# Kernel optimization log

Hardware: AMD Instinct MI355X
Metric: run time of the kernel (lower is better)

The kernel has to match this reference:

```python
import jax, jax.numpy as jnp
import numpy as np

N_HEAD = 8
DROP_RATE = 0.1


def setup_inputs() -> dict:
    key = jax.random.key(0)
    k1, k2, k3 = jax.random.split(key, 3)
    n, c, h, w = 16, 512, 32, 32
    return {
        "x": jax.random.normal(k1, (n, c, h, w), jnp.float32),
        "qkv_w": jax.random.normal(k2, (3 * c, c), jnp.float32) * 0.02,
        "qkv_b": jnp.zeros((3 * c,), jnp.float32),
        "out_w": jax.random.normal(k3, (c, c), jnp.float32) * 0.02,
        "out_b": jnp.zeros((c,), jnp.float32),
        "dropout_enabled": 0,
    }


def reference(x, qkv_w, qkv_b, out_w, out_b, dropout_enabled):
    n, c, h, w = x.shape
    hd = c // N_HEAD  # head dim
    # fused QKV 1x1 conv == per-pixel matmul: [n, 3c, h, w]
    qkv = jnp.einsum('oc,nchw->nohw', qkv_w, x) + qkv_b[None, :, None, None]
    # [n, 3*n_head, hd, h*w] -> [n, 3*n_head, h*w, hd]
    qkv = jnp.swapaxes(qkv.reshape(n, N_HEAD * 3, hd, h * w), 2, 3)
    q, k, v = jnp.split(qkv, 3, axis=1)  # each [n, n_head, hw, hd]
    scale = hd ** (-0.25)
    att = jax.nn.softmax((q * scale) @ (jnp.swapaxes(k, 2, 3) * scale), axis=3)
    y = jnp.swapaxes(att @ v, 2, 3).reshape(n, c, h, w)
    y = jnp.einsum('oc,nchw->nohw', out_w, y) + out_b[None, :, None, None]
    # Dropout2d: drops whole (n, c) channel maps
    rate = DROP_RATE * dropout_enabled
    keep = jax.random.bernoulli(jax.random.key(42), 1.0 - rate, shape=(n, c))
    y = y * keep[..., None, None] / (1.0 - rate)
    return x + y
```

## Files before the change

### kernel.cpp

```cpp
#include <hip/hip_runtime.h>

typedef short bf16x8 __attribute__((ext_vector_type(8)));
typedef float f32x4 __attribute__((ext_vector_type(4)));
typedef float f32x16 __attribute__((ext_vector_type(16)));

#define MFMA16(a,b,c) __builtin_amdgcn_mfma_f32_16x16x32_bf16((a),(b),(c),0,0,0)
#define MFMA32(a,b,c) __builtin_amdgcn_mfma_f32_32x32x16_bf16((a),(b),(c),0,0,0)

static __device__ __forceinline__ unsigned short f2bf(float f){
  unsigned u; __builtin_memcpy(&u, &f, 4);
  u += 0x7fffu + ((u >> 16) & 1u);
  return (unsigned short)(u >> 16);
}

static __device__ __forceinline__ unsigned cvtpk(float lo, float hi){
  unsigned r;
  asm volatile("v_cvt_pk_bf16_f32 %0, %1, %2" : "=v"(r) : "v"(lo), "v"(hi));
  return r;
}
static __device__ __forceinline__ void pl32swap(unsigned &a, unsigned &b){
  asm volatile("v_permlane32_swap_b32 %0, %1" : "+v"(a), "+v"(b));
}

static __device__ __forceinline__ void gload_lds16(const void* g, void* l) {
  __builtin_amdgcn_global_load_lds(
      (__attribute__((address_space(1))) void*)g,
      (__attribute__((address_space(3))) void*)l, 16, 0, 0);
}

__global__ __launch_bounds__(256) void cvt_w(
    const float* __restrict__ qkv_w, const float* __restrict__ out_w,
    unsigned short* __restrict__ wq, unsigned short* __restrict__ wo) {
  int i = blockIdx.x * 256 + threadIdx.x;
  if (i < 786432) wq[i] = f2bf(qkv_w[i]);
  else            wo[i - 786432] = f2bf(out_w[i - 786432]);
}

__global__ __launch_bounds__(256) void transpose_cvt(
    const float* __restrict__ in, unsigned short* __restrict__ out)
{
  __shared__ unsigned short tile[32][33];
  const long base = (long)blockIdx.z * 512 * 1024;
  const int t = threadIdx.x, tx = t & 31, ty = t >> 5;
  const int c0 = blockIdx.x * 32, r0 = blockIdx.y * 32;
  const float* ib = in + base;
#pragma unroll
  for (int i = 0; i < 4; ++i)
    tile[ty + i * 8][tx] = f2bf(ib[(long)(r0 + ty + i * 8) * 1024 + c0 + tx]);
  __syncthreads();
  unsigned short* ob = out + base;
#pragma unroll
  for (int i = 0; i < 4; ++i)
    ob[(long)(c0 + ty + i * 8) * 512 + r0 + tx] = tile[tx][ty + i * 8];
}

__global__ __launch_bounds__(256, 2) void gemm_qkv(
    const unsigned short* __restrict__ A, const unsigned short* __restrict__ B,
    unsigned short* __restrict__ qkvout, const float* __restrict__ bias)
{
  const int M = 1024, K = 512;
  __shared__ unsigned short SM[4][128 * 64];
  const int t = threadIdx.x, lane = t & 63, wv = t >> 6;
  const int quad = lane >> 4, ln = lane & 15;

  const int L = blockIdx.x + 12 * blockIdx.y + 96 * blockIdx.z;
  const int v = (L & 7) * 192 + (L >> 3);
  const int m0 = ((v / 12) & 7) * 128, n0 = (v % 12) * 128;
  const long zb = v / 96;
  A += zb * (long)M * K;

  const int srow = wv * 32 + (lane >> 3);
  const int scol = ((lane & 7) * 8) ^ ((lane >> 3) * 8);

  auto stage = [&](int kt, unsigned short* Ad, unsigned short* Bd) {
#pragma unroll
    for (int i = 0; i < 4; ++i) {
      gload_lds16(&A[(long)(m0 + srow + i * 8) * K + kt + scol],
                  &Ad[(wv * 32 + i * 8) * 64]);
      gload_lds16(&B[(long)(n0 + srow + i * 8) * K + kt + scol],
                  &Bd[(wv * 32 + i * 8) * 64]);
    }
  };

  f32x4 zero = {0.f, 0.f, 0.f, 0.f};
  f32x4 acc[4][4];
#pragma unroll
  for (int i = 0; i < 4; ++i)
#pragma unroll
    for (int j = 0; j < 4; ++j) acc[i][j] = zero;

  const int wm = (wv & 1) * 64, wn = (wv >> 1) * 64;
  const int rsw = (ln & 7) * 8;

  stage(0, SM[0], SM[2]);
  for (int kt8 = 0; kt8 < 8; ++kt8) {
    const int cur = kt8 & 1;
    if (kt8 < 7) {
      stage((kt8 + 1) * 64, SM[cur ^ 1], SM[2 + (cur ^ 1)]);
      asm volatile("s_waitcnt vmcnt(8)" ::: "memory");
    } else {
      asm volatile("s_waitcnt vmcnt(0)" ::: "memory");
    }
    __builtin_amdgcn_s_barrier();
    const unsigned short* As = SM[cur];
    const unsigned short* Bs = SM[2 + cur];
#pragma unroll
    for (int kk = 0; kk < 64; kk += 32) {
      bf16x8 a[4], b[4];
#pragma unroll
      for (int i = 0; i < 4; ++i)
        a[i] = *(const bf16x8*)&As[(wm + i * 16 + ln) * 64 + ((kk + quad * 8) ^ rsw)];
#pragma unroll
      for (int j = 0; j < 4; ++j)
        b[j] = *(const bf16x8*)&Bs[(wn + j * 16 + ln) * 64 + ((kk + quad * 8) ^ rsw)];
#pragma unroll
      for (int i = 0; i < 4; ++i)
#pragma unroll
        for (int j = 0; j < 4; ++j)
          acc[i][j] = MFMA16(a[i], b[j], acc[i][j]);
    }
    __builtin_amdgcn_s_barrier();
  }

  const int part = n0 >> 9;
  if (part < 2) {
    const float qs = (part == 0) ? 0.18033688f : 1.0f;
    unsigned short (*T)[136] = (unsigned short(*)[136])&SM[0][0];
    __syncthreads();
#pragma unroll
    for (int j = 0; j < 4; ++j) {
      const int oo = wn + j * 16 + ln;
      const float bb = bias[n0 + oo];
#pragma unroll
      for (int i = 0; i < 4; ++i) {
        const int pp = wm + i * 16 + quad * 4;
        f32x4 vv = acc[i][j];
#pragma unroll
        for (int r = 0; r < 4; ++r)
          T[pp + r][oo] = f2bf((vv[r] + bb) * qs);
      }
    }
    __syncthreads();
    unsigned short* qb = qkvout + (long)part * 8388608;
#pragma unroll
    for (int it = 0; it < 8; ++it) {
      const int idx = it * 256 + t;
      const int p = idx >> 4, c0 = (idx & 15) * 8;
      const int og = n0 + c0;
      const int h = (og >> 6) & 7, d = og & 63;
      bf16x8 val = *(const bf16x8*)&T[p][c0];
      *(bf16x8*)&qb[((long)(zb * 8 + h) * 1024 + m0 + p) * 64 + d] = val;
    }
  } else {
#pragma unroll
    for (int j = 0; j < 4; ++j) {
      const int o = n0 + wn + j * 16 + ln;
      const float bb = bias[o];
#pragma unroll
      for (int i = 0; i < 4; ++i) {
        const int p = m0 + wm + i * 16 + quad * 4;
        const long cidx = ((long)zb * 512 + (o - 1024)) * 1024 + p;
        f32x4 vv = acc[i][j];
        ushort4 st;
        st.x = f2bf(vv[0] + bb); st.y = f2bf(vv[1] + bb);
        st.z = f2bf(vv[2] + bb); st.w = f2bf(vv[3] + bb);
        *(ushort4*)&qkvout[16777216 + cidx] = st;
      }
    }
  }
}

__global__ __launch_bounds__(256, 2) void gemm_out(
    const unsigned short* __restrict__ A, const unsigned short* __restrict__ B,
    float* __restrict__ C, const float* __restrict__ bias,
    const float* __restrict__ xin, const int* __restrict__ de_ptr)
{
  const int M = 1024, K = 512;
  __shared__ unsigned short SM[4][128 * 64];
  const int t = threadIdx.x, lane = t & 63, wv = t >> 6;
  const int quad = lane >> 4, ln = lane & 15;

  const int L = blockIdx.x + 4 * blockIdx.y + 32 * blockIdx.z;
  const int v = (L & 7) * 64 + (L >> 3);
  const int m0 = ((v >> 2) & 7) * 128, n0 = (v & 3) * 128;
  const long zb = v >> 5;
  A += zb * (long)M * K;
  C += zb * 512l * M;
  xin += zb * 512l * M;

  const int srow = wv * 32 + (lane >> 3);
  const int scol = ((lane & 7) * 8) ^ ((lane >> 3) * 8);

  auto stage = [&](int kt, unsigned short* Ad, unsigned short* Bd) {
#pragma unroll
    for (int i = 0; i < 4; ++i) {
      gload_lds16(&A[(long)(m0 + srow + i * 8) * K + kt + scol],
                  &Ad[(wv * 32 + i * 8) * 64]);
      gload_lds16(&B[(long)(n0 + srow + i * 8) * K + kt + scol],
                  &Bd[(wv * 32 + i * 8) * 64]);
    }
  };

  f32x4 zero = {0.f, 0.f, 0.f, 0.f};
  f32x4 acc[4][4];
#pragma unroll
  for (int i = 0; i < 4; ++i)
#pragma unroll
    for (int j = 0; j < 4; ++j) acc[i][j] = zero;

  const int wm = (wv & 1) * 64, wn = (wv >> 1) * 64;
  const int rsw = (ln & 7) * 8;

  stage(0, SM[0], SM[2]);
  for (int kt8 = 0; kt8 < 8; ++kt8) {
    const int cur = kt8 & 1;
    if (kt8 < 7) {
      stage((kt8 + 1) * 64, SM[cur ^ 1], SM[2 + (cur ^ 1)]);
      asm volatile("s_waitcnt vmcnt(8)" ::: "memory");
    } else {
      asm volatile("s_waitcnt vmcnt(0)" ::: "memory");
    }
    __builtin_amdgcn_s_barrier();
    const unsigned short* As = SM[cur];
    const unsigned short* Bs = SM[2 + cur];
#pragma unroll
    for (int kk = 0; kk < 64; kk += 32) {
      bf16x8 a[4], b[4];
#pragma unroll
      for (int i = 0; i < 4; ++i)
        a[i] = *(const bf16x8*)&As[(wm + i * 16 + ln) * 64 + ((kk + quad * 8) ^ rsw)];
#pragma unroll
      for (int j = 0; j < 4; ++j)
        b[j] = *(const bf16x8*)&Bs[(wn + j * 16 + ln) * 64 + ((kk + quad * 8) ^ rsw)];
#pragma unroll
      for (int i = 0; i < 4; ++i)
#pragma unroll
        for (int j = 0; j < 4; ++j)
          acc[i][j] = MFMA16(a[i], b[j], acc[i][j]);
    }
    __builtin_amdgcn_s_barrier();
  }

  float dscale = 1.0f / (1.0f - 0.1f * (float)de_ptr[0]);

#pragma unroll
  for (int j = 0; j < 4; ++j) {
    int o = n0 + wn + j * 16 + ln;
    float bb = bias[o];
#pragma unroll
    for (int i = 0; i < 4; ++i) {
      int p = m0 + wm + i * 16 + quad * 4;
      long cidx = (long)o * M + p;
      f32x4 vv = acc[i][j];
      float4 rx = *(const float4*)&xin[cidx];
      float4 st;
      st.x = rx.x + (vv[0] + bb) * dscale;
      st.y = rx.y + (vv[1] + bb) * dscale;
      st.z = rx.z + (vv[2] + bb) * dscale;
      st.w = rx.w + (vv[3] + bb) * dscale;
      *(float4*)&C[cidx] = st;
    }
  }
}

__global__ __launch_bounds__(512, 2) void attn_kernel(
    const unsigned short* __restrict__ q_pd, const unsigned short* __restrict__ k_pd,
    const unsigned short* __restrict__ v_cp, unsigned short* __restrict__ y_pc)
{
  __shared__ unsigned short Ks[3][128 * 64];
  __shared__ unsigned short Vs[3][64 * 128];
  const int t = threadIdx.x, lane = t & 63, wv = t >> 6;
  const int l31 = lane & 31, bh8 = (lane >> 5) * 8;
  const int qt = blockIdx.y >> 5;
  const int nh = blockIdx.x * 32 + (blockIdx.y & 31);
  const int n = nh >> 3, h = nh & 7;
  const int q0 = qt * 512;

  bf16x8 qa[2][4];
#pragma unroll
  for (int qg = 0; qg < 2; ++qg) {
    const unsigned short* qb =
        q_pd + ((long)nh * 1024 + q0 + wv * 64 + qg * 32 + l31) * 64;
#pragma unroll
    for (int ds = 0; ds < 4; ++ds)
      qa[qg][ds] = *(const bf16x8*)(qb + ds * 16 + bh8);
  }

  f32x16 zacc;
#pragma unroll
  for (int r = 0; r < 16; ++r) zacc[r] = 0.f;
  f32x16 o_acc[2][2];
  o_acc[0][0] = zacc; o_acc[0][1] = zacc; o_acc[1][0] = zacc; o_acc[1][1] = zacc;
  float l_acc[2] = {0.f, 0.f};

  const unsigned short* kg0 = k_pd + (long)nh * 1024 * 64;
  const unsigned short* vg0 = v_cp + ((long)n * 512 + h * 64) * 1024;

  const int krow = lane >> 3;
  const int kcol = ((lane & 7) * 8) ^ ((lane >> 3) * 8);
  const int vrow = lane >> 4;
  const int rsw = (lane & 7) * 8;
  const int vrsw = (l31 & 15) * 8;

  auto stage_kv = [&](int c, int buf) {
    const unsigned short* kg = kg0 + (long)c * 128 * 64;
    const unsigned short* vg = vg0 + c * 128;
    unsigned short* KsD = Ks[buf];
    unsigned short* VsD = Vs[buf];
#pragma unroll
    for (int i = 0; i < 2; ++i) {
      const int vr = ((wv & 1) * 8) + i * 4 + vrow;
      const int vcol = ((lane & 15) ^ vr) * 8;
      gload_lds16(kg + (long)(wv * 16 + i * 8 + krow) * 64 + kcol,
                  &KsD[(wv * 16 + i * 8) * 64]);
      gload_lds16(vg + (long)(wv * 8 + i * 4 + vrow) * 1024 + vcol,
                  &VsD[(wv * 8 + i * 4) * 128]);
    }
  };

  stage_kv(0, 0);
  stage_kv(1, 1);

  union U { bf16x8 v; unsigned u[4]; };
  auto sm_pack = [&](const f32x16& sv, bf16x8* paq, float& lac) {
    float e[16];
#pragma unroll
    for (int r = 0; r < 16; ++r) e[r] = __builtin_amdgcn_exp2f(sv[r]);
    float ls = 0.f;
#pragma unroll
    for (int r = 0; r < 16; ++r) ls += e[r];
    lac += ls;
    unsigned pk4[4][2];
#pragma unroll
    for (int hh = 0; hh < 4; ++hh) {
      pk4[hh][0] = cvtpk(e[4 * hh + 0], e[4 * hh + 1]);
      pk4[hh][1] = cvtpk(e[4 * hh + 2], e[4 * hh + 3]);
    }
#pragma unroll
    for (int hk = 0; hk < 2; ++hk) {
      unsigned a0 = pk4[2 * hk + 1][0], b0 = pk4[2 * hk][0];
      unsigned a1 = pk4[2 * hk + 1][1], b1 = pk4[2 * hk][1];
      pl32swap(a0, b0); pl32swap(a1, b1);
      U u; u.u[0] = b0; u.u[1] = b1; u.u[2] = a0; u.u[3] = a1;
      paq[hk] = u.v;
    }
  };

  for (int c = 0; c < 8; ++c) {
    const int cur = c % 3;
    if (c < 6) {
      stage_kv(c + 2, (c + 2) % 3);
      asm volatile("s_waitcnt vmcnt(8)" ::: "memory");
    } else if (c == 6) {
      asm volatile("s_waitcnt vmcnt(4)" ::: "memory");
    } else {
      asm volatile("s_waitcnt vmcnt(0)" ::: "memory");
    }
    __builtin_amdgcn_s_barrier();
    const unsigned short* KsC = Ks[cur];
    const unsigned short* VsC = Vs[cur];

#pragma unroll
    for (int kgi = 0; kgi < 4; ++kgi) {
      f32x16 s0 = zacc, s1 = zacc;
      __builtin_amdgcn_s_setprio(1);
#pragma unroll
      for (int ds = 0; ds < 4; ++ds) {
        bf16x8 ka = *(const bf16x8*)&KsC[(kgi * 32 + l31) * 64 + ((ds * 16 + bh8) ^ rsw)];
        s0 = MFMA32(ka, qa[0][ds], s0);
        s1 = MFMA32(ka, qa[1][ds], s1);
      }
      __builtin_amdgcn_s_setprio(0);
      bf16x8 pa[2][2];
      sm_pack(s0, pa[0], l_acc[0]);
      sm_pack(s1, pa[1], l_acc[1]);
      __builtin_amdgcn_s_setprio(1);
#pragma unroll
      for (int dg = 0; dg < 2; ++dg)
#pragma unroll
        for (int hk = 0; hk < 2; ++hk) {
          bf16x8 va = *(const bf16x8*)
              &VsC[(dg * 32 + l31) * 128 + (((kgi * 2 + hk) * 16 + bh8) ^ vrsw)];
          o_acc[dg][0] = MFMA32(va, pa[0][hk], o_acc[dg][0]);
          o_acc[dg][1] = MFMA32(va, pa[1][hk], o_acc[dg][1]);
        }
      __builtin_amdgcn_s_setprio(0);
    }
    __builtin_amdgcn_s_barrier();
  }

#pragma unroll
  for (int qg = 0; qg < 2; ++qg) {
    float la = l_acc[qg];
    la += __shfl_xor(la, 32);
    float linv = 1.0f / la;
    const int q = q0 + wv * 64 + qg * 32 + l31;
    unsigned short* yb = y_pc + ((long)n * 1024 + q) * 512 + h * 64;
#pragma unroll
    for (int dg = 0; dg < 2; ++dg) {
      f32x16 o = o_acc[dg][qg];
#pragma unroll
      for (int rq = 0; rq < 4; ++rq) {
        int d0 = dg * 32 + rq * 8 + (bh8 >> 1);
        ushort4 st;
        st.x = f2bf(o[rq * 4 + 0] * linv);
        st.y = f2bf(o[rq * 4 + 1] * linv);
        st.z = f2bf(o[rq * 4 + 2] * linv);
        st.w = f2bf(o[rq * 4 + 3] * linv);
        *(ushort4*)&yb[d0] = st;
      }
    }
  }
}

extern "C" void kernel_launch(void* const* d_in, const int* in_sizes, int n_in,
                              void* d_out, int out_size, void* d_ws, size_t ws_size,
                              hipStream_t stream) {
  (void)in_sizes; (void)n_in; (void)out_size; (void)ws_size;
  const float* x     = (const float*)d_in[0];
  const float* qkv_w = (const float*)d_in[1];
  const float* qkv_b = (const float*)d_in[2];
  const float* out_w = (const float*)d_in[3];
  const float* out_b = (const float*)d_in[4];
  const int* de = (const int*)d_in[5];
  float* out = (float*)d_out;
  unsigned short* ws = (unsigned short*)d_ws;

  unsigned short* xT   = ws;
  unsigned short* qkv  = ws + 8388608;
  unsigned short* y_pc = ws;
  unsigned short* wq   = ws + 33554432;
  unsigned short* wo   = wq + 786432;

  cvt_w<<<4096, 256, 0, stream>>>(qkv_w, out_w, wq, wo);

  transpose_cvt<<<dim3(32, 16, 16), 256, 0, stream>>>(x, xT);

  gemm_qkv<<<dim3(12, 8, 16), 256, 0, stream>>>(xT, wq, qkv, qkv_b);

  attn_kernel<<<dim3(4, 64), 512, 0, stream>>>(
      qkv, qkv + 8388608, qkv + 16777216, y_pc);

  gemm_out<<<dim3(4, 8, 16), 256, 0, stream>>>(
      y_pc, wo, out, out_b, x, de);
}
```

Measured before the change: 198.8 us.

## Double-buffer attention K/V, batch QK MFMAs, simplify GEMM prefetch sync

The GEMM kernels replace manual vmcnt waits plus raw barriers with __syncthreads around a double-buffered prefetch, and drop a redundant sync before the epilogue. The attention kernel goes from triple to double buffering of K/V tiles, which cuts LDS per block and may let two 512-thread blocks fit per CU. It also processes two 32-key groups at once: it hoists K and V fragment loads ahead of the MFMA chains and interleaves independent accumulators. The softmax row sum becomes a tree reduction. In exchange, prefetch depth is shorter, so load latency is less hidden, and register pressure rises.

After: 199.8 us. No clear change (+0.5%).

```diff
diff --git a/kernel.cpp b/kernel.cpp
--- a/kernel.cpp
+++ b/kernel.cpp
@@ -93,15 +93,10 @@
   const int rsw = (ln & 7) * 8;
 
   stage(0, SM[0], SM[2]);
+  __syncthreads();
   for (int kt8 = 0; kt8 < 8; ++kt8) {
     const int cur = kt8 & 1;
-    if (kt8 < 7) {
-      stage((kt8 + 1) * 64, SM[cur ^ 1], SM[2 + (cur ^ 1)]);
-      asm volatile("s_waitcnt vmcnt(8)" ::: "memory");
-    } else {
-      asm volatile("s_waitcnt vmcnt(0)" ::: "memory");
-    }
-    __builtin_amdgcn_s_barrier();
+    if (kt8 < 7) stage((kt8 + 1) * 64, SM[cur ^ 1], SM[2 + (cur ^ 1)]);
     const unsigned short* As = SM[cur];
     const unsigned short* Bs = SM[2 + cur];
 #pragma unroll
@@ -119,14 +114,13 @@
         for (int j = 0; j < 4; ++j)
           acc[i][j] = MFMA16(a[i], b[j], acc[i][j]);
     }
-    __builtin_amdgcn_s_barrier();
+    __syncthreads();
   }
 
   const int part = n0 >> 9;
   if (part < 2) {
     const float qs = (part == 0) ? 0.18033688f : 1.0f;
     unsigned short (*T)[136] = (unsigned short(*)[136])&SM[0][0];
-    __syncthreads();
 #pragma unroll
     for (int j = 0; j < 4; ++j) {
       const int oo = wn + j * 16 + ln;
@@ -212,15 +206,10 @@
   const int rsw = (ln & 7) * 8;
 
   stage(0, SM[0], SM[2]);
+  __syncthreads();
   for (int kt8 = 0; kt8 < 8; ++kt8) {
     const int cur = kt8 & 1;
-    if (kt8 < 7) {
-      stage((kt8 + 1) * 64, SM[cur ^ 1], SM[2 + (cur ^ 1)]);
-      asm volatile("s_waitcnt vmcnt(8)" ::: "memory");
-    } else {
-      asm volatile("s_waitcnt vmcnt(0)" ::: "memory");
-    }
-    __builtin_amdgcn_s_barrier();
+    if (kt8 < 7) stage((kt8 + 1) * 64, SM[cur ^ 1], SM[2 + (cur ^ 1)]);
     const unsigned short* As = SM[cur];
     const unsigned short* Bs = SM[2 + cur];
 #pragma unroll
@@ -238,7 +227,7 @@
         for (int j = 0; j < 4; ++j)
           acc[i][j] = MFMA16(a[i], b[j], acc[i][j]);
     }
-    __builtin_amdgcn_s_barrier();
+    __syncthreads();
   }
 
   float dscale = 1.0f / (1.0f - 0.1f * (float)de_ptr[0]);
@@ -267,8 +256,8 @@
     const unsigned short* __restrict__ q_pd, const unsigned short* __restrict__ k_pd,
     const unsigned short* __restrict__ v_cp, unsigned short* __restrict__ y_pc)
 {
-  __shared__ unsigned short Ks[3][128 * 64];
-  __shared__ unsigned short Vs[3][64 * 128];
+  __shared__ unsigned short Ks[2][128 * 64];
+  __shared__ unsigned short Vs[2][64 * 128];
   const int t = threadIdx.x, lane = t & 63, wv = t >> 6;
   const int l31 = lane & 31, bh8 = (lane >> 5) * 8;
   const int qt = blockIdx.y >> 5;
@@ -319,17 +308,16 @@
   };
 
   stage_kv(0, 0);
-  stage_kv(1, 1);
 
   union U { bf16x8 v; unsigned u[4]; };
   auto sm_pack = [&](const f32x16& sv, bf16x8* paq, float& lac) {
     float e[16];
 #pragma unroll
     for (int r = 0; r < 16; ++r) e[r] = __builtin_amdgcn_exp2f(sv[r]);
-    float ls = 0.f;
-#pragma unroll
-    for (int r = 0; r < 16; ++r) ls += e[r];
-    lac += ls;
+    float a0 = e[0] + e[1],  a1 = e[2] + e[3],  a2 = e[4] + e[5],  a3 = e[6] + e[7];
+    float a4 = e[8] + e[9],  a5 = e[10] + e[11], a6 = e[12] + e[13], a7 = e[14] + e[15];
+    float b0 = a0 + a1, b1 = a2 + a3, b2 = a4 + a5, b3 = a6 + a7;
+    lac += (b0 + b1) + (b2 + b3);
     unsigned pk4[4][2];
 #pragma unroll
     for (int hh = 0; hh < 4; ++hh) {
@@ -338,20 +326,18 @@
     }
 #pragma unroll
     for (int hk = 0; hk < 2; ++hk) {
-      unsigned a0 = pk4[2 * hk + 1][0], b0 = pk4[2 * hk][0];
-      unsigned a1 = pk4[2 * hk + 1][1], b1 = pk4[2 * hk][1];
-      pl32swap(a0, b0); pl32swap(a1, b1);
-      U u; u.u[0] = b0; u.u[1] = b1; u.u[2] = a0; u.u[3] = a1;
+      unsigned x0 = pk4[2 * hk + 1][0], y0 = pk4[2 * hk][0];
+      unsigned x1 = pk4[2 * hk + 1][1], y1 = pk4[2 * hk][1];
+      pl32swap(x0, y0); pl32swap(x1, y1);
+      U u; u.u[0] = y0; u.u[1] = y1; u.u[2] = x0; u.u[3] = x1;
       paq[hk] = u.v;
     }
   };
 
   for (int c = 0; c < 8; ++c) {
-    const int cur = c % 3;
-    if (c < 6) {
-      stage_kv(c + 2, (c + 2) % 3);
-      asm volatile("s_waitcnt vmcnt(8)" ::: "memory");
-    } else if (c == 6) {
+    const int cur = c & 1;
+    if (c < 7) {
+      stage_kv(c + 1, cur ^ 1);
       asm volatile("s_waitcnt vmcnt(4)" ::: "memory");
     } else {
       asm volatile("s_waitcnt vmcnt(0)" ::: "memory");
@@ -361,30 +347,47 @@
     const unsigned short* VsC = Vs[cur];
 
 #pragma unroll
-    for (int kgi = 0; kgi < 4; ++kgi) {
-      f32x16 s0 = zacc, s1 = zacc;
+    for (int g = 0; g < 2; ++g) {
+      bf16x8 ka[2][4];
+#pragma unroll
+      for (int kk = 0; kk < 2; ++kk)
+#pragma unroll
+        for (int ds = 0; ds < 4; ++ds)
+          ka[kk][ds] = *(const bf16x8*)
+              &KsC[((g * 2 + kk) * 32 + l31) * 64 + ((ds * 16 + bh8) ^ rsw)];
+      f32x16 s[2][2];
+      s[0][0] = zacc; s[0][1] = zacc; s[1][0] = zacc; s[1][1] = zacc;
       __builtin_amdgcn_s_setprio(1);
 #pragma unroll
-      for (int ds = 0; ds < 4; ++ds) {
-        bf16x8 ka = *(const bf16x8*)&KsC[(kgi * 32 + l31) * 64 + ((ds * 16 + bh8) ^ rsw)];
-        s0 = MFMA32(ka, qa[0][ds], s0);
-        s1 = MFMA32(ka, qa[1][ds], s1);
-      }
-      __builtin_amdgcn_s_setprio(0);
-      bf16x8 pa[2][2];
-      sm_pack(s0, pa[0], l_acc[0]);
-      sm_pack(s1, pa[1], l_acc[1]);
-      __builtin_amdgcn_s_setprio(1);
-#pragma unroll
-      for (int dg = 0; dg < 2; ++dg)
-#pragma unroll
-        for (int hk = 0; hk < 2; ++hk) {
-          bf16x8 va = *(const bf16x8*)
-              &VsC[(dg * 32 + l31) * 128 + (((kgi * 2 + hk) * 16 + bh8) ^ vrsw)];
-          o_acc[dg][0] = MFMA32(va, pa[0][hk], o_acc[dg][0]);
-          o_acc[dg][1] = MFMA32(va, pa[1][hk], o_acc[dg][1]);
+      for (int ds = 0; ds < 4; ++ds)
+#pragma unroll
+        for (int kk = 0; kk < 2; ++kk) {
+          s[kk][0] = MFMA32(ka[kk][ds], qa[0][ds], s[kk][0]);
+          s[kk][1] = MFMA32(ka[kk][ds], qa[1][ds], s[kk][1]);
         }
       __builtin_amdgcn_s_setprio(0);
+#pragma unroll
+      for (int kk = 0; kk < 2; ++kk) {
+        bf16x8 va[4];
+#pragma unroll
+        for (int dg = 0; dg < 2; ++dg)
+#pragma unroll
+          for (int hk = 0; hk < 2; ++hk)
+            va[dg * 2 + hk] = *(const bf16x8*)
+                &VsC[(dg * 32 + l31) * 128 + ((((g * 2 + kk) * 2 + hk) * 16 + bh8) ^ vrsw)];
+        bf16x8 pa[2][2];
+        sm_pack(s[kk][0], pa[0], l_acc[0]);
+        sm_pack(s[kk][1], pa[1], l_acc[1]);
+        __builtin_amdgcn_s_setprio(1);
+#pragma unroll
+        for (int dg = 0; dg < 2; ++dg)
+#pragma unroll
+          for (int hk = 0; hk < 2; ++hk) {
+            o_acc[dg][0] = MFMA32(va[dg * 2 + hk], pa[0][hk], o_acc[dg][0]);
+            o_acc[dg][1] = MFMA32(va[dg * 2 + hk], pa[1][hk], o_acc[dg][1]);
+          }
+        __builtin_amdgcn_s_setprio(0);
+      }
     }
     __builtin_amdgcn_s_barrier();
   }
```
